# Kernel optimization log

Hardware: AMD Instinct MI355X
Metric: run time of the kernel (lower is better)

Reference implementation:

```python
import jax, jax.numpy as jnp
import numpy as np

B, S, IN, OUT = 4, 512, 512, 112

def setup_inputs() -> dict:
    key = jax.random.key(0)
    k1, k2, k3, k4 = jax.random.split(key, 4)
    input1 = jax.random.normal(k1, (B, S, IN), dtype=jnp.float32)
    input2 = jax.random.normal(k2, (B, S, IN), dtype=jnp.float32)
    # xavier-uniform-ish init scales
    lim1 = float(np.sqrt(6.0 / (IN + IN)))
    w1 = jax.random.uniform(k3, (IN, OUT, IN), dtype=jnp.float32, minval=-lim1, maxval=lim1)
    lim2 = float(np.sqrt(6.0 / (2 * IN + 1 + OUT)))
    w2 = jax.random.uniform(k4, (2 * IN + 1, OUT), dtype=jnp.float32, minval=-lim2, maxval=lim2)
    return {"input1": input1, "input2": input2, "w1": w1, "w2": w2, "seq_len": S}

def reference(input1, input2, w1, w2, seq_len):
    in_size = input1.shape[-1]
    # Biaffine trilinear term: [B, S, S, OUT]
    logits_1 = jnp.einsum('bxi,ioj,byj->bxyo', input1, w1, input2)
    # Concat-linear term without materializing the [B,S,S,2*IN+1] tensor.
    # Original concatenates (input1 broadcast over y, input1 broadcast over x, ones):
    # note BOTH halves come from input1, faithful to the source code.
    wA = w2[:in_size]          # acts on f1 = input1[b, x]
    wB = w2[in_size:2 * in_size]  # acts on f2 = input1[b, y]
    bias = w2[2 * in_size]     # acts on the appended ones
    termA = jnp.einsum('bxi,io->bxo', input1, wA)  # [B,S,OUT]
    termB = jnp.einsum('byi,io->byo', input1, wB)  # [B,S,OUT]
    logits_2 = termA[:, :, None, :] + termB[:, None, :, :] + bias
    return logits_1 + logits_2
```

## Files before the change

kernel.cpp:

```cpp
#include <hip/hip_runtime.h>
#include <cstdint>

constexpr int B_    = 4;
constexpr int S_    = 512;
constexpr int IN_   = 512;
constexpr int OUT_  = 112;
constexpr int NROW_ = B_ * S_;
constexpr int NN_   = OUT_ * IN_;
constexpr int K_    = IN_;

typedef __attribute__((ext_vector_type(8))) short          s16x8;
typedef __attribute__((ext_vector_type(4))) float          f32x4;
typedef __attribute__((ext_vector_type(8))) unsigned short u16x8;
typedef __attribute__((ext_vector_type(4))) unsigned short u16x4;

__device__ __forceinline__ unsigned short f2bf(float f) {
  union { float f; unsigned u; } v; v.f = f;
  unsigned u = v.u;
  return (unsigned short)((u + 0x7FFFu + ((u >> 16) & 1u)) >> 16);
}

__device__ __forceinline__ void gld_lds16(const void* g, void* l) {
  __builtin_amdgcn_global_load_lds(
      (const __attribute__((address_space(1))) unsigned int*)(unsigned long long)g,
      (__attribute__((address_space(3))) unsigned int*)(unsigned int)(unsigned long long)l,
      16, 0, 0);
}

__global__ __launch_bounds__(256) void cast_kernel(
    const float* __restrict__ in1, const float* __restrict__ in2,
    unsigned short* __restrict__ in1b, unsigned short* __restrict__ in2b) {
  int idx = blockIdx.x * 256 + threadIdx.x;
  float4 v1 = ((const float4*)in1)[idx];
  float4 v2 = ((const float4*)in2)[idx];
  ((u16x4*)in1b)[idx] = (u16x4){f2bf(v1.x), f2bf(v1.y), f2bf(v1.z), f2bf(v1.w)};
  ((u16x4*)in2b)[idx] = (u16x4){f2bf(v2.x), f2bf(v2.y), f2bf(v2.z), f2bf(v2.w)};
}

__global__ __launch_bounds__(256) void transpose_w1(
    const float* __restrict__ w1, unsigned short* __restrict__ w1T) {
  __shared__ unsigned short tile[64][40];
  const int t  = threadIdx.x;
  const int n0 = blockIdx.x * 64;
  const int i0 = blockIdx.y * 32;
#pragma unroll
  for (int p = 0; p < 8; ++p) {
    int il = p * 4 + (t >> 6);
    int nl = t & 63;
    tile[nl][il] = f2bf(w1[(size_t)(i0 + il) * NN_ + n0 + nl]);
  }
  __syncthreads();
  int nl = t >> 2, ch = t & 3;
  u16x8 v = *(const u16x8*)&tile[nl][ch * 8];
  *(u16x8*)&w1T[(size_t)(n0 + nl) * K_ + i0 + ch * 8] = v;
}

__global__ __launch_bounds__(128) void term_kernel(
    const float* __restrict__ in1, const float* __restrict__ w2,
    float* __restrict__ termA, float* __restrict__ termB) {
  const int bx = blockIdx.x;
  const int o  = threadIdx.x;
  if (o >= OUT_) return;
  const float* row = in1 + (size_t)bx * IN_;
  float a = 0.f, c = 0.f;
  for (int i = 0; i < IN_; ++i) {
    float v = row[i];
    a += v * w2[i * OUT_ + o];
    c += v * w2[(IN_ + i) * OUT_ + o];
  }
  termA[bx * OUT_ + o] = a + w2[2 * IN_ * OUT_ + o];
  termB[bx * OUT_ + o] = c;
}

__global__ __launch_bounds__(256) void gemm1_kernel(
    const unsigned short* __restrict__ A,
    const unsigned short* __restrict__ Bm,
    unsigned short* __restrict__ U) {
  __shared__ unsigned short As[128 * 32];
  __shared__ unsigned short Bs[128 * 32];
  const int tid = threadIdx.x;
  const int wid = tid >> 6, lane = tid & 63;
  const int wm = wid & 1, wn = wid >> 1;
  const int m0 = blockIdx.x * 128;
  const int n0 = blockIdx.y * 128;
  const int rl0 = wid * 16 + (lane >> 2);
  const int rl1 = rl0 + 64;
  const int kcol = lane & 3;

  const unsigned short* aP0 = A + (size_t)(m0 + rl0) * K_ + kcol * 8;
  const unsigned short* aP1 = A + (size_t)(m0 + rl1) * K_ + kcol * 8;
  const unsigned short* bP0 = Bm + (size_t)(n0 + rl0) * K_ + kcol * 8;
  const unsigned short* bP1 = Bm + (size_t)(n0 + rl1) * K_ + kcol * 8;
  unsigned short* lA0 = &As[rl0 * 32 + kcol * 8];
  unsigned short* lA1 = &As[rl1 * 32 + kcol * 8];
  unsigned short* lB0 = &Bs[rl0 * 32 + kcol * 8];
  unsigned short* lB1 = &Bs[rl1 * 32 + kcol * 8];

  const int ln = lane & 15, q = lane >> 4;
  f32x4 acc[4][4];
#pragma unroll
  for (int i = 0; i < 4; ++i)
#pragma unroll
    for (int j = 0; j < 4; ++j) acc[i][j] = (f32x4){0.f, 0.f, 0.f, 0.f};

  for (int kt = 0; kt < K_ / 32; ++kt) {
    gld_lds16(aP0, lA0); gld_lds16(aP1, lA1);
    gld_lds16(bP0, lB0); gld_lds16(bP1, lB1);
    aP0 += 32; aP1 += 32; bP0 += 32; bP1 += 32;
    __syncthreads();
    s16x8 af[4], bfr[4];
#pragma unroll
    for (int mf = 0; mf < 4; ++mf)
      af[mf] = *(const s16x8*)&As[(wm * 64 + mf * 16 + ln) * 32 + q * 8];
#pragma unroll
    for (int nf = 0; nf < 4; ++nf)
      bfr[nf] = *(const s16x8*)&Bs[(wn * 64 + nf * 16 + ln) * 32 + q * 8];
#pragma unroll
    for (int mf = 0; mf < 4; ++mf)
#pragma unroll
      for (int nf = 0; nf < 4; ++nf)
        acc[mf][nf] = __builtin_amdgcn_mfma_f32_16x16x32_bf16(af[mf], bfr[nf], acc[mf][nf], 0, 0, 0);
    __syncthreads();
  }
#pragma unroll
  for (int mf = 0; mf < 4; ++mf) {
    const int mrow = m0 + wm * 64 + mf * 16 + q * 4;
#pragma unroll
    for (int nf = 0; nf < 4; ++nf) {
      const int ncol = n0 + wn * 64 + nf * 16 + ln;
#pragma unroll
      for (int r = 0; r < 4; ++r)
        U[(size_t)(mrow + r) * NN_ + ncol] = f2bf(acc[mf][nf][r]);
    }
  }
}

__global__ __launch_bounds__(256) void gemm2_kernel(
    const unsigned short* __restrict__ A,
    const unsigned short* __restrict__ U,
    const float* __restrict__ termA,
    const float* __restrict__ termB,
    float* __restrict__ out) {
  __shared__ unsigned short As[128 * 32];
  __shared__ unsigned short Bs[128 * 32];
  const int tid = threadIdx.x;
  const int wid = tid >> 6, lane = tid & 63;
  const int wm = wid & 1, wn = wid >> 1;
  const int b  = blockIdx.z;
  const int m0 = blockIdx.x * 128;
  const int n0 = blockIdx.y * 128;
  const int rl0 = wid * 16 + (lane >> 2);
  const int rl1 = rl0 + 64;
  const int kcol = lane & 3;

  const unsigned short* aP0 = A + (size_t)(b * S_ + m0 + rl0) * K_ + kcol * 8;
  const unsigned short* aP1 = A + (size_t)(b * S_ + m0 + rl1) * K_ + kcol * 8;
  const int r2 = n0 + rl0, x0r = r2 / OUT_, o0r = r2 - x0r * OUT_;
  const int r3 = n0 + rl1, x1r = r3 / OUT_, o1r = r3 - x1r * OUT_;
  const unsigned short* bP0 = U + (size_t)(b * S_ + x0r) * NN_ + o0r * K_ + kcol * 8;
  const unsigned short* bP1 = U + (size_t)(b * S_ + x1r) * NN_ + o1r * K_ + kcol * 8;
  unsigned short* lA0 = &As[rl0 * 32 + kcol * 8];
  unsigned short* lA1 = &As[rl1 * 32 + kcol * 8];
  unsigned short* lB0 = &Bs[rl0 * 32 + kcol * 8];
  unsigned short* lB1 = &Bs[rl1 * 32 + kcol * 8];

  const int ln = lane & 15, q = lane >> 4;
  f32x4 acc[4][4];
#pragma unroll
  for (int i = 0; i < 4; ++i)
#pragma unroll
    for (int j = 0; j < 4; ++j) acc[i][j] = (f32x4){0.f, 0.f, 0.f, 0.f};

  for (int kt = 0; kt < K_ / 32; ++kt) {
    gld_lds16(aP0, lA0); gld_lds16(aP1, lA1);
    gld_lds16(bP0, lB0); gld_lds16(bP1, lB1);
    aP0 += 32; aP1 += 32; bP0 += 32; bP1 += 32;
    __syncthreads();
    s16x8 af[4], bfr[4];
#pragma unroll
    for (int mf = 0; mf < 4; ++mf)
      af[mf] = *(const s16x8*)&As[(wm * 64 + mf * 16 + ln) * 32 + q * 8];
#pragma unroll
    for (int nf = 0; nf < 4; ++nf)
      bfr[nf] = *(const s16x8*)&Bs[(wn * 64 + nf * 16 + ln) * 32 + q * 8];
#pragma unroll
    for (int mf = 0; mf < 4; ++mf)
#pragma unroll
      for (int nf = 0; nf < 4; ++nf)
        acc[mf][nf] = __builtin_amdgcn_mfma_f32_16x16x32_bf16(af[mf], bfr[nf], acc[mf][nf], 0, 0, 0);
    __syncthreads();
  }

#pragma unroll
  for (int nf = 0; nf < 4; ++nf) {
    const int n = n0 + wn * 64 + nf * 16 + ln;
    const int x = n / OUT_, o = n - x * OUT_;
    const float tA = termA[b * NN_ + n];
    const float* tB = termB + b * NN_ + o;
    float* op = out + ((size_t)(b * S_ + x) * S_) * OUT_ + o;
#pragma unroll
    for (int mf = 0; mf < 4; ++mf) {
      const int y0 = m0 + wm * 64 + mf * 16 + q * 4;
#pragma unroll
      for (int r = 0; r < 4; ++r) {
        const int y = y0 + r;
        op[(size_t)y * OUT_] = acc[mf][nf][r] + tA + tB[y * OUT_];
      }
    }
  }
}

extern "C" void kernel_launch(void* const* d_in, const int* in_sizes, int n_in,
                              void* d_out, int out_size, void* d_ws, size_t ws_size,
                              hipStream_t stream) {
  const float* in1 = (const float*)d_in[0];
  const float* in2 = (const float*)d_in[1];
  const float* w1  = (const float*)d_in[2];
  const float* w2  = (const float*)d_in[3];
  float* out = (float*)d_out;

  char* ws = (char*)d_ws;
  size_t off = 0;
  unsigned short* w1T  = (unsigned short*)(ws + off); off += (size_t)NN_ * K_ * 2;
  unsigned short* U    = (unsigned short*)(ws + off); off += (size_t)NROW_ * NN_ * 2;
  unsigned short* in1b = (unsigned short*)(ws + off); off += (size_t)NROW_ * IN_ * 2;
  unsigned short* in2b = (unsigned short*)(ws + off); off += (size_t)NROW_ * IN_ * 2;
  float* termA = (float*)(ws + off); off += (size_t)NROW_ * OUT_ * 4;
  float* termB = (float*)(ws + off); off += (size_t)NROW_ * OUT_ * 4;
  if (ws_size < off) return;

  cast_kernel<<<(NROW_ * IN_ / 4) / 256, 256, 0, stream>>>(in1, in2, in1b, in2b);
  transpose_w1<<<dim3(NN_ / 64, K_ / 32), 256, 0, stream>>>(w1, w1T);
  term_kernel<<<NROW_, 128, 0, stream>>>(in1, w2, termA, termB);
  gemm1_kernel<<<dim3(NROW_ / 128, NN_ / 128), 256, 0, stream>>>(in1b, w1T, U);
  gemm2_kernel<<<dim3(S_ / 128, NN_ / 128, B_), 256, 0, stream>>>(in2b, U, termA, termB, out);
}
```

Measured before the change: 1.016 ms.

## Double-buffer LDS tiles and remap block indices for XCD-aware L2 locality

Both GEMM kernels now use double-buffered shared memory, so the next K-tile's global-to-LDS load is issued before the current tile's MFMAs, with explicit vmcnt/lgkmcnt waits and barriers in place of two __syncthreads per step. The grids are flattened to 1D and blockIdx is remapped so that each XCD (bid & 7) processes a contiguous panel of N tiles across all M tiles. This is meant to improve L2 reuse of the shared operand. The cost is twice the LDS per block, which may lower occupancy, and hand-tuned wait counts that depend on exact load ordering.

```diff
diff --git a/kernel.cpp b/kernel.cpp
--- a/kernel.cpp
+++ b/kernel.cpp
@@ -76,13 +76,19 @@
     const unsigned short* __restrict__ A,
     const unsigned short* __restrict__ Bm,
     unsigned short* __restrict__ U) {
-  __shared__ unsigned short As[128 * 32];
-  __shared__ unsigned short Bs[128 * 32];
+  __shared__ unsigned short As[2][128 * 32];
+  __shared__ unsigned short Bs[2][128 * 32];
   const int tid = threadIdx.x;
   const int wid = tid >> 6, lane = tid & 63;
   const int wm = wid & 1, wn = wid >> 1;
-  const int m0 = blockIdx.x * 128;
-  const int n0 = blockIdx.y * 128;
+
+  const int d   = blockIdx.x;
+  const int xcd = d & 7, kk = d >> 3;
+  const int pan = xcd * 56 + (kk >> 4);
+  const int mi  = kk & 15;
+  const int m0  = mi * 128;
+  const int n0  = pan * 128;
+
   const int rl0 = wid * 16 + (lane >> 2);
   const int rl1 = rl0 + 64;
   const int kcol = lane & 3;
@@ -91,10 +97,8 @@
   const unsigned short* aP1 = A + (size_t)(m0 + rl1) * K_ + kcol * 8;
   const unsigned short* bP0 = Bm + (size_t)(n0 + rl0) * K_ + kcol * 8;
   const unsigned short* bP1 = Bm + (size_t)(n0 + rl1) * K_ + kcol * 8;
-  unsigned short* lA0 = &As[rl0 * 32 + kcol * 8];
-  unsigned short* lA1 = &As[rl1 * 32 + kcol * 8];
-  unsigned short* lB0 = &Bs[rl0 * 32 + kcol * 8];
-  unsigned short* lB1 = &Bs[rl1 * 32 + kcol * 8];
+  const int la0 = rl0 * 32 + kcol * 8;
+  const int la1 = rl1 * 32 + kcol * 8;
 
   const int ln = lane & 15, q = lane >> 4;
   f32x4 acc[4][4];
@@ -103,24 +107,37 @@
 #pragma unroll
     for (int j = 0; j < 4; ++j) acc[i][j] = (f32x4){0.f, 0.f, 0.f, 0.f};
 
-  for (int kt = 0; kt < K_ / 32; ++kt) {
-    gld_lds16(aP0, lA0); gld_lds16(aP1, lA1);
-    gld_lds16(bP0, lB0); gld_lds16(bP1, lB1);
+  auto stage = [&](int bb) {
+    gld_lds16(aP0, &As[bb][la0]); gld_lds16(aP1, &As[bb][la1]);
+    gld_lds16(bP0, &Bs[bb][la0]); gld_lds16(bP1, &Bs[bb][la1]);
     aP0 += 32; aP1 += 32; bP0 += 32; bP1 += 32;
-    __syncthreads();
+  };
+
+  constexpr int NT = K_ / 32;
+  stage(0);
+  for (int kt = 0; kt < NT; ++kt) {
+    const int cur = kt & 1;
+    if (kt < NT - 1) {
+      stage(cur ^ 1);
+      asm volatile("s_waitcnt vmcnt(4)" ::: "memory");
+    } else {
+      asm volatile("s_waitcnt vmcnt(0)" ::: "memory");
+    }
+    __builtin_amdgcn_s_barrier();
     s16x8 af[4], bfr[4];
 #pragma unroll
     for (int mf = 0; mf < 4; ++mf)
-      af[mf] = *(const s16x8*)&As[(wm * 64 + mf * 16 + ln) * 32 + q * 8];
+      af[mf] = *(const s16x8*)&As[cur][(wm * 64 + mf * 16 + ln) * 32 + q * 8];
 #pragma unroll
     for (int nf = 0; nf < 4; ++nf)
-      bfr[nf] = *(const s16x8*)&Bs[(wn * 64 + nf * 16 + ln) * 32 + q * 8];
+      bfr[nf] = *(const s16x8*)&Bs[cur][(wn * 64 + nf * 16 + ln) * 32 + q * 8];
+    asm volatile("s_waitcnt lgkmcnt(0)" ::: "memory");
+    __builtin_amdgcn_s_barrier();
 #pragma unroll
     for (int mf = 0; mf < 4; ++mf)
 #pragma unroll
       for (int nf = 0; nf < 4; ++nf)
         acc[mf][nf] = __builtin_amdgcn_mfma_f32_16x16x32_bf16(af[mf], bfr[nf], acc[mf][nf], 0, 0, 0);
-    __syncthreads();
   }
 #pragma unroll
   for (int mf = 0; mf < 4; ++mf) {
@@ -141,14 +158,21 @@
     const float* __restrict__ termA,
     const float* __restrict__ termB,
     float* __restrict__ out) {
-  __shared__ unsigned short As[128 * 32];
-  __shared__ unsigned short Bs[128 * 32];
+  __shared__ unsigned short As[2][128 * 32];
+  __shared__ unsigned short Bs[2][128 * 32];
   const int tid = threadIdx.x;
   const int wid = tid >> 6, lane = tid & 63;
   const int wm = wid & 1, wn = wid >> 1;
-  const int b  = blockIdx.z;
-  const int m0 = blockIdx.x * 128;
-  const int n0 = blockIdx.y * 128;
+
+  const int d   = blockIdx.x;
+  const int xcd = d & 7, kk = d >> 3;
+  const int pan = xcd * 224 + (kk >> 2);
+  const int mi  = kk & 3;
+  const int b   = pan / 448;
+  const int ni  = pan - b * 448;
+  const int m0  = mi * 128;
+  const int n0  = ni * 128;
+
   const int rl0 = wid * 16 + (lane >> 2);
   const int rl1 = rl0 + 64;
   const int kcol = lane & 3;
@@ -159,10 +183,8 @@
   const int r3 = n0 + rl1, x1r = r3 / OUT_, o1r = r3 - x1r * OUT_;
   const unsigned short* bP0 = U + (size_t)(b * S_ + x0r) * NN_ + o0r * K_ + kcol * 8;
   const unsigned short* bP1 = U + (size_t)(b * S_ + x1r) * NN_ + o1r * K_ + kcol * 8;
-  unsigned short* lA0 = &As[rl0 * 32 + kcol * 8];
-  unsigned short* lA1 = &As[rl1 * 32 + kcol * 8];
-  unsigned short* lB0 = &Bs[rl0 * 32 + kcol * 8];
-  unsigned short* lB1 = &Bs[rl1 * 32 + kcol * 8];
+  const int la0 = rl0 * 32 + kcol * 8;
+  const int la1 = rl1 * 32 + kcol * 8;
 
   const int ln = lane & 15, q = lane >> 4;
   f32x4 acc[4][4];
@@ -171,24 +193,37 @@
 #pragma unroll
     for (int j = 0; j < 4; ++j) acc[i][j] = (f32x4){0.f, 0.f, 0.f, 0.f};
 
-  for (int kt = 0; kt < K_ / 32; ++kt) {
-    gld_lds16(aP0, lA0); gld_lds16(aP1, lA1);
-    gld_lds16(bP0, lB0); gld_lds16(bP1, lB1);
+  auto stage = [&](int bb) {
+    gld_lds16(aP0, &As[bb][la0]); gld_lds16(aP1, &As[bb][la1]);
+    gld_lds16(bP0, &Bs[bb][la0]); gld_lds16(bP1, &Bs[bb][la1]);
     aP0 += 32; aP1 += 32; bP0 += 32; bP1 += 32;
-    __syncthreads();
+  };
+
+  constexpr int NT = K_ / 32;
+  stage(0);
+  for (int kt = 0; kt < NT; ++kt) {
+    const int cur = kt & 1;
+    if (kt < NT - 1) {
+      stage(cur ^ 1);
+      asm volatile("s_waitcnt vmcnt(4)" ::: "memory");
+    } else {
+      asm volatile("s_waitcnt vmcnt(0)" ::: "memory");
+    }
+    __builtin_amdgcn_s_barrier();
     s16x8 af[4], bfr[4];
 #pragma unroll
     for (int mf = 0; mf < 4; ++mf)
-      af[mf] = *(const s16x8*)&As[(wm * 64 + mf * 16 + ln) * 32 + q * 8];
+      af[mf] = *(const s16x8*)&As[cur][(wm * 64 + mf * 16 + ln) * 32 + q * 8];
 #pragma unroll
     for (int nf = 0; nf < 4; ++nf)
-      bfr[nf] = *(const s16x8*)&Bs[(wn * 64 + nf * 16 + ln) * 32 + q * 8];
+      bfr[nf] = *(const s16x8*)&Bs[cur][(wn * 64 + nf * 16 + ln) * 32 + q * 8];
+    asm volatile("s_waitcnt lgkmcnt(0)" ::: "memory");
+    __builtin_amdgcn_s_barrier();
 #pragma unroll
     for (int mf = 0; mf < 4; ++mf)
 #pragma unroll
       for (int nf = 0; nf < 4; ++nf)
         acc[mf][nf] = __builtin_amdgcn_mfma_f32_16x16x32_bf16(af[mf], bfr[nf], acc[mf][nf], 0, 0, 0);
-    __syncthreads();
   }
 
 #pragma unroll
@@ -232,6 +267,6 @@
   cast_kernel<<<(NROW_ * IN_ / 4) / 256, 256, 0, stream>>>(in1, in2, in1b, in2b);
   transpose_w1<<<dim3(NN_ / 64, K_ / 32), 256, 0, stream>>>(w1, w1T);
   term_kernel<<<NROW_, 128, 0, stream>>>(in1, w2, termA, termB);
-  gemm1_kernel<<<dim3(NROW_ / 128, NN_ / 128), 256, 0, stream>>>(in1b, w1T, U);
-  gemm2_kernel<<<dim3(S_ / 128, NN_ / 128, B_), 256, 0, stream>>>(in2b, U, termA, termB, out);
-}
+  gemm1_kernel<<<7168, 256, 0, stream>>>(in1b, w1T, U);
+  gemm2_kernel<<<7168, 256, 0, stream>>>(in2b, U, termA, termB, out);
+}
```

New measurement: 1.016 ms. About the same (+0.1%).
